# Optimization experiments

Hardware: AMD Instinct MI355X
Metric: run time of the kernel (lower is better)

Reference implementation:

```python
import jax, jax.numpy as jnp
import numpy as np

QUALITY = 75

Y_TABLE = np.array([
    [16, 11, 10, 16, 24, 40, 51, 61],
    [12, 12, 14, 19, 26, 58, 60, 55],
    [14, 13, 16, 24, 40, 57, 69, 56],
    [14, 17, 22, 29, 51, 87, 80, 62],
    [18, 22, 37, 56, 68, 109, 103, 77],
    [24, 35, 55, 64, 81, 104, 113, 92],
    [49, 64, 78, 87, 103, 121, 120, 101],
    [72, 92, 95, 98, 112, 100, 103, 99]], dtype=np.float32)

C_TABLE = np.array([
    [17, 18, 24, 47, 99, 99, 99, 99],
    [18, 21, 26, 66, 99, 99, 99, 99],
    [24, 26, 56, 99, 99, 99, 99, 99],
    [47, 66, 99, 99, 99, 99, 99, 99],
    [99, 99, 99, 99, 99, 99, 99, 99],
    [99, 99, 99, 99, 99, 99, 99, 99],
    [99, 99, 99, 99, 99, 99, 99, 99],
    [99, 99, 99, 99, 99, 99, 99, 99]], dtype=np.float32)

def _dct_mat():
    # Orthonormal 8-point DCT-II matrix D: coef = D @ block @ D.T
    xg = np.arange(8, dtype=np.float64)
    ug = np.arange(8, dtype=np.float64)
    D = 0.5 * np.cos((2.0 * xg[None, :] + 1.0) * ug[:, None] * np.pi / 16.0)
    D[0, :] *= 1.0 / np.sqrt(2.0)
    return jnp.asarray(D, dtype=jnp.float32)

D8 = _dct_mat()

def _blockify(ch):
    # [B,H,W] -> [B, H//8, W//8, 8, 8]
    B, H, W = ch.shape
    return ch.reshape(B, H // 8, 8, W // 8, 8).transpose(0, 1, 3, 2, 4)

def _deblockify(blk):
    # [B, hb, wb, 8, 8] -> [B, hb*8, wb*8]
    B, hb, wb, _, _ = blk.shape
    return blk.transpose(0, 1, 3, 2, 4).reshape(B, hb * 8, wb * 8)

def _channel_jpeg(ch, table, factor):
    # ch: [B,H,W] in 0..255 -> quantize/dequantize in DCT domain
    q = table * factor  # [8,8]
    blk = _blockify(ch - 128.0)                                   # [B,hb,wb,8,8]
    coef = jnp.einsum('bhwxy,ux,vy->bhwuv', blk, D8, D8)           # 8x8 DCT
    coef = jnp.round(coef / q) * q                                 # quantize + dequantize
    rec = jnp.einsum('bhwuv,ux,vy->bhwxy', coef, D8, D8) + 128.0   # IDCT
    return _deblockify(rec)

def jpeg_compress(img, quality):
    # img: [B,3,H,W] in [0,1]
    if quality < 50:
        factor = 5000.0 / quality
    else:
        factor = 200.0 - 2.0 * quality
    factor = factor / 100.0
    x = img * 255.0
    r, g, b = x[:, 0], x[:, 1], x[:, 2]
    y = 0.299 * r + 0.587 * g + 0.114 * b
    cb = -0.168736 * r - 0.331264 * g + 0.5 * b + 128.0
    cr = 0.5 * r - 0.418688 * g - 0.081312 * b + 128.0
    # 4:2:0 chroma subsampling via 2x2 average pooling
    B, H, W = cb.shape
    cb_s = cb.reshape(B, H // 2, 2, W // 2, 2).mean(axis=(2, 4))
    cr_s = cr.reshape(B, H // 2, 2, W // 2, 2).mean(axis=(2, 4))
    y_r = _channel_jpeg(y, jnp.asarray(Y_TABLE), factor)
    cb_r = _channel_jpeg(cb_s, jnp.asarray(C_TABLE), factor)
    cr_r = _channel_jpeg(cr_s, jnp.asarray(C_TABLE), factor)
    # nearest-neighbor chroma upsampling
    cb_u = jnp.repeat(jnp.repeat(cb_r, 2, axis=1), 2, axis=2)
    cr_u = jnp.repeat(jnp.repeat(cr_r, 2, axis=1), 2, axis=2)
    cbm = cb_u - 128.0
    crm = cr_u - 128.0
    r2 = y_r + 1.402 * crm
    g2 = y_r - 0.344136 * cbm - 0.714136 * crm
    b2 = y_r + 1.772 * cbm
    out = jnp.stack([r2, g2, b2], axis=1)
    return jnp.clip(out, 0.0, 255.0) / 255.0


def setup_inputs() -> dict:
    key = jax.random.key(0)
    x = jax.random.uniform(key, (16, 3, 512, 512), dtype=jnp.float32)
    return {"x": x}


def reference(x):
    img_clip = jnp.clip(x, 0.0, 1.0)
    img_jpeg = jpeg_compress(img_clip, QUALITY)
    img_gap = jax.lax.stop_gradient(img_jpeg - x)
    return x + img_gap
```

## Files before the change

### kernel.cpp

```cpp
#include <hip/hip_runtime.h>
#include <math.h>

#define CH_STRIDE (512 * 512)

static constexpr float DMc[8][8] = {
  { 0.35355339059327373f, 0.35355339059327373f, 0.35355339059327373f, 0.35355339059327373f,
    0.35355339059327373f, 0.35355339059327373f, 0.35355339059327373f, 0.35355339059327373f},
  { 0.49039264020161522f, 0.41573480615127262f, 0.27778511650980111f, 0.09754516100806413f,
   -0.09754516100806413f,-0.27778511650980111f,-0.41573480615127262f,-0.49039264020161522f},
  { 0.46193976625564337f, 0.19134171618254489f,-0.19134171618254489f,-0.46193976625564337f,
   -0.46193976625564337f,-0.19134171618254489f, 0.19134171618254489f, 0.46193976625564337f},
  { 0.41573480615127262f,-0.09754516100806413f,-0.49039264020161522f,-0.27778511650980111f,
    0.27778511650980111f, 0.49039264020161522f, 0.09754516100806413f,-0.41573480615127262f},
  { 0.35355339059327373f,-0.35355339059327373f,-0.35355339059327373f, 0.35355339059327373f,
    0.35355339059327373f,-0.35355339059327373f,-0.35355339059327373f, 0.35355339059327373f},
  { 0.27778511650980111f,-0.49039264020161522f, 0.09754516100806413f, 0.41573480615127262f,
   -0.41573480615127262f,-0.09754516100806413f, 0.49039264020161522f,-0.27778511650980111f},
  { 0.19134171618254489f,-0.46193976625564337f, 0.46193976625564337f,-0.19134171618254489f,
   -0.19134171618254489f, 0.46193976625564337f,-0.46193976625564337f, 0.19134171618254489f},
  { 0.09754516100806413f,-0.27778511650980111f, 0.41573480615127262f,-0.49039264020161522f,
    0.49039264020161522f,-0.41573480615127262f, 0.27778511650980111f,-0.09754516100806413f},
};

static constexpr float QTABc[128] = {
   8.0f,  5.5f,  5.0f,  8.0f, 12.0f, 20.0f, 25.5f, 30.5f,
   6.0f,  6.0f,  7.0f,  9.5f, 13.0f, 29.0f, 30.0f, 27.5f,
   7.0f,  6.5f,  8.0f, 12.0f, 20.0f, 28.5f, 34.5f, 28.0f,
   7.0f,  8.5f, 11.0f, 14.5f, 25.5f, 43.5f, 40.0f, 31.0f,
   9.0f, 11.0f, 18.5f, 28.0f, 34.0f, 54.5f, 51.5f, 38.5f,
  12.0f, 17.5f, 27.5f, 32.0f, 40.5f, 52.0f, 56.5f, 46.0f,
  24.5f, 32.0f, 39.0f, 43.5f, 51.5f, 60.5f, 60.0f, 50.5f,
  36.0f, 46.0f, 47.5f, 49.0f, 56.0f, 50.0f, 51.5f, 49.5f,

   8.5f,  9.0f, 12.0f, 23.5f, 49.5f, 49.5f, 49.5f, 49.5f,
   9.0f, 10.5f, 13.0f, 33.0f, 49.5f, 49.5f, 49.5f, 49.5f,
  12.0f, 13.0f, 28.0f, 49.5f, 49.5f, 49.5f, 49.5f, 49.5f,
  23.5f, 33.0f, 49.5f, 49.5f, 49.5f, 49.5f, 49.5f, 49.5f,
  49.5f, 49.5f, 49.5f, 49.5f, 49.5f, 49.5f, 49.5f, 49.5f,
  49.5f, 49.5f, 49.5f, 49.5f, 49.5f, 49.5f, 49.5f, 49.5f,
  49.5f, 49.5f, 49.5f, 49.5f, 49.5f, 49.5f, 49.5f, 49.5f,
  49.5f, 49.5f, 49.5f, 49.5f, 49.5f, 49.5f, 49.5f, 49.5f,
};

__device__ __forceinline__ float fm(float a, float b) { return __fmul_rn(a, b); }
__device__ __forceinline__ float fa(float a, float b) { return __fadd_rn(a, b); }
__device__ __forceinline__ float fs(float a, float b) { return __fsub_rn(a, b); }
__device__ __forceinline__ float fd(float a, float b) { return __fdiv_rn(a, b); }

__global__ __launch_bounds__(256, 2)
void jpeg_kernel(const float* __restrict__ x, float* __restrict__ out) {
  const int lane = threadIdx.x & 63;
  const int wave = threadIdx.x >> 6;

  const int q  = blockIdx.x;
  const int b  = q >> 8;
  const int qq = q & 255;
  const int ty = ((qq >> 4) << 1) + (wave >> 1);
  const int tx = ((qq & 15) << 1) + (wave & 1);
  const int row0 = ty << 4, col0 = tx << 4;

  __shared__ __align__(16) float Ytile[4][16][20];
  __shared__ __align__(16) float CbRaw[4][16][17];
  __shared__ __align__(16) float CrRaw[4][16][17];
  __shared__ __align__(16) float CbBlk[4][8][9];
  __shared__ __align__(16) float CrBlk[4][8][9];
  __shared__ __align__(16) float Cq[4][6][8][9];
  __shared__ __align__(16) float CbR[4][8][9];
  __shared__ __align__(16) float CrR[4][8][9];

  const int pr  = lane >> 2;
  const int pcq = lane & 3;
  const int pc  = pcq << 2;
  const size_t ibase = ((((size_t)b * 3) * 512 + (row0 + pr)) * 512) + (size_t)(col0 + pc);

  float4 rv = *(const float4*)(x + ibase);
  float4 gv = *(const float4*)(x + ibase + CH_STRIDE);
  float4 bv = *(const float4*)(x + ibase + 2 * CH_STRIDE);
  float xr[4] = {rv.x, rv.y, rv.z, rv.w};
  float xg[4] = {gv.x, gv.y, gv.z, gv.w};
  float xb[4] = {bv.x, bv.y, bv.z, bv.w};

#pragma unroll
  for (int i = 0; i < 4; ++i) {
    float r  = fm(fminf(fmaxf(xr[i], 0.0f), 1.0f), 255.0f);
    float g  = fm(fminf(fmaxf(xg[i], 0.0f), 1.0f), 255.0f);
    float bb = fm(fminf(fmaxf(xb[i], 0.0f), 1.0f), 255.0f);
    float y  = fa(fa(fm(0.299f, r), fm(0.587f, g)), fm(0.114f, bb));
    Ytile[wave][pr][pc + i] = fs(y, 128.0f);
    float cb = fa(fa(fs(fm(-0.168736f, r), fm(0.331264f, g)), fm(0.5f, bb)), 128.0f);
    CbRaw[wave][pr][pc + i] = cb;
    float cr = fa(fs(fs(fm(0.5f, r), fm(0.418688f, g)), fm(0.081312f, bb)), 128.0f);
    CrRaw[wave][pr][pc + i] = cr;
  }
  __syncthreads();

  {
    const int i = lane >> 3, j = lane & 7;
    {
      float c00 = CbRaw[wave][2 * i][2 * j],     c01 = CbRaw[wave][2 * i][2 * j + 1];
      float c10 = CbRaw[wave][2 * i + 1][2 * j], c11 = CbRaw[wave][2 * i + 1][2 * j + 1];
      CbBlk[wave][i][j] = fs(fd(fa(fa(c00, c01), fa(c10, c11)), 4.0f), 128.0f);
    }
    {
      float c00 = CrRaw[wave][2 * i][2 * j],     c01 = CrRaw[wave][2 * i][2 * j + 1];
      float c10 = CrRaw[wave][2 * i + 1][2 * j], c11 = CrRaw[wave][2 * i + 1][2 * j + 1];
      CrBlk[wave][i][j] = fs(fd(fa(fa(c00, c01), fa(c10, c11)), 4.0f), 128.0f);
    }
  }
  __syncthreads();

  const bool act = lane < 48;
  const int g = lane >> 3;
  const int j = lane & 7;
  const int rb  = (g >> 1) << 3;
  const int cb0 = (g & 1) << 3;

  if (act) {
    float t0[64];
    if (g < 4) {
#pragma unroll
      for (int xx = 0; xx < 8; ++xx)
#pragma unroll
        for (int yy = 0; yy < 8; ++yy)
          t0[xx * 8 + yy] = fm(Ytile[wave][rb + xx][cb0 + yy], DMc[j][xx]);
    } else if (g == 4) {
#pragma unroll
      for (int xx = 0; xx < 8; ++xx)
#pragma unroll
        for (int yy = 0; yy < 8; ++yy)
          t0[xx * 8 + yy] = fm(CbBlk[wave][xx][yy], DMc[j][xx]);
    } else {
#pragma unroll
      for (int xx = 0; xx < 8; ++xx)
#pragma unroll
        for (int yy = 0; yy < 8; ++yy)
          t0[xx * 8 + yy] = fm(CrBlk[wave][xx][yy], DMc[j][xx]);
    }

    const float* qr = QTABc + ((g < 4) ? 0 : 64) + j * 8;
#pragma unroll
    for (int v = 0; v < 8; ++v) {
      float s0 = 0.0f, s1 = 0.0f, s2 = 0.0f, s3 = 0.0f;
#pragma unroll
      for (int m = 0; m < 16; ++m) {
        const int k = 4 * m;
        s0 = fa(s0, fm(t0[k + 0], DMc[v][(k + 0) & 7]));
        s1 = fa(s1, fm(t0[k + 1], DMc[v][(k + 1) & 7]));
        s2 = fa(s2, fm(t0[k + 2], DMc[v][(k + 2) & 7]));
        s3 = fa(s3, fm(t0[k + 3], DMc[v][(k + 3) & 7]));
      }
      float coef = fa(fa(s0, s1), fa(s2, s3));
      float qv = qr[v];
      Cq[wave][g][j][v] = fm(rintf(fd(coef, qv)), qv);
    }
  }
  __syncthreads();

  if (act) {
    float t2[64];
#pragma unroll
    for (int u = 0; u < 8; ++u)
#pragma unroll
      for (int v = 0; v < 8; ++v)
        t2[u * 8 + v] = fm(Cq[wave][g][u][v], DMc[u][j]);

#pragma unroll
    for (int yy = 0; yy < 8; ++yy) {
      float acc = 0.0f;
#pragma unroll
      for (int u = 0; u < 8; ++u)
#pragma unroll
        for (int v = 0; v < 8; ++v)
          acc = fa(acc, fm(t2[u * 8 + v], DMc[v][yy]));
      float rec = fa(acc, 128.0f);
      if (g < 4) {
        Ytile[wave][rb + j][cb0 + yy] = rec;
      } else if (g == 4) {
        CbR[wave][j][yy] = fs(rec, 128.0f);
      } else {
        CrR[wave][j][yy] = fs(rec, 128.0f);
      }
    }
  }
  __syncthreads();

  float ro[4], go[4], bo[4];
#pragma unroll
  for (int i = 0; i < 4; ++i) {
    float y_r = Ytile[wave][pr][pc + i];
    float cbm = CbR[wave][pr >> 1][(pc + i) >> 1];
    float crm = CrR[wave][pr >> 1][(pc + i) >> 1];
    float r2 = fa(y_r, fm(1.402f, crm));
    float g2 = fs(fs(y_r, fm(0.344136f, cbm)), fm(0.714136f, crm));
    float b2 = fa(y_r, fm(1.772f, cbm));
    float jr = fd(fminf(fmaxf(r2, 0.0f), 255.0f), 255.0f);
    float jg = fd(fminf(fmaxf(g2, 0.0f), 255.0f), 255.0f);
    float jb = fd(fminf(fmaxf(b2, 0.0f), 255.0f), 255.0f);
    ro[i] = fa(xr[i], fs(jr, xr[i]));
    go[i] = fa(xg[i], fs(jg, xg[i]));
    bo[i] = fa(xb[i], fs(jb, xb[i]));
  }
  *(float4*)(out + ibase)                 = make_float4(ro[0], ro[1], ro[2], ro[3]);
  *(float4*)(out + ibase + CH_STRIDE)     = make_float4(go[0], go[1], go[2], go[3]);
  *(float4*)(out + ibase + 2 * CH_STRIDE) = make_float4(bo[0], bo[1], bo[2], bo[3]);
}

extern "C" void kernel_launch(void* const* d_in, const int* in_sizes, int n_in,
                              void* d_out, int out_size, void* d_ws, size_t ws_size,
                              hipStream_t stream) {
  const float* x = (const float*)d_in[0];
  float* out = (float*)d_out;
  jpeg_kernel<<<dim3(4096), dim3(256), 0, stream>>>(x, out);
}
```

Measured before the change: 131.9 us.

## Restructure JPEG kernel to block-wide 32x32 tiles with register-light DCT

Each 256-thread block now handles one 32x32 tile cooperatively instead of four independent 16x16 wave tiles. Chroma subsampling is done with cross-lane shuffles, which removes the raw-chroma shared buffers and one barrier. The DCT and IDCT loops are restructured to stream rows with float4 LDS reads and keep small accumulators instead of 64-element arrays, which lowers register pressure so launch bounds can target four blocks per CU. The input is re-read from global memory in the epilogue rather than held in registers across barriers, adding some memory traffic in exchange for lower register use.

```diff
diff --git a/kernel.cpp b/kernel.cpp
--- a/kernel.cpp
+++ b/kernel.cpp
@@ -47,162 +47,177 @@
 __device__ __forceinline__ float fs(float a, float b) { return __fsub_rn(a, b); }
 __device__ __forceinline__ float fd(float a, float b) { return __fdiv_rn(a, b); }
 
-__global__ __launch_bounds__(256, 2)
+__global__ __launch_bounds__(256, 4)
 void jpeg_kernel(const float* __restrict__ x, float* __restrict__ out) {
-  const int lane = threadIdx.x & 63;
-  const int wave = threadIdx.x >> 6;
-
+  const int tid = threadIdx.x;
   const int q  = blockIdx.x;
   const int b  = q >> 8;
   const int qq = q & 255;
-  const int ty = ((qq >> 4) << 1) + (wave >> 1);
-  const int tx = ((qq & 15) << 1) + (wave & 1);
-  const int row0 = ty << 4, col0 = tx << 4;
-
-  __shared__ __align__(16) float Ytile[4][16][20];
-  __shared__ __align__(16) float CbRaw[4][16][17];
-  __shared__ __align__(16) float CrRaw[4][16][17];
-  __shared__ __align__(16) float CbBlk[4][8][9];
-  __shared__ __align__(16) float CrBlk[4][8][9];
-  __shared__ __align__(16) float Cq[4][6][8][9];
-  __shared__ __align__(16) float CbR[4][8][9];
-  __shared__ __align__(16) float CrR[4][8][9];
-
-  const int pr  = lane >> 2;
-  const int pcq = lane & 3;
-  const int pc  = pcq << 2;
-  const size_t ibase = ((((size_t)b * 3) * 512 + (row0 + pr)) * 512) + (size_t)(col0 + pc);
-
-  float4 rv = *(const float4*)(x + ibase);
-  float4 gv = *(const float4*)(x + ibase + CH_STRIDE);
-  float4 bv = *(const float4*)(x + ibase + 2 * CH_STRIDE);
-  float xr[4] = {rv.x, rv.y, rv.z, rv.w};
-  float xg[4] = {gv.x, gv.y, gv.z, gv.w};
-  float xb[4] = {bv.x, bv.y, bv.z, bv.w};
-
-#pragma unroll
-  for (int i = 0; i < 4; ++i) {
-    float r  = fm(fminf(fmaxf(xr[i], 0.0f), 1.0f), 255.0f);
-    float g  = fm(fminf(fmaxf(xg[i], 0.0f), 1.0f), 255.0f);
-    float bb = fm(fminf(fmaxf(xb[i], 0.0f), 1.0f), 255.0f);
-    float y  = fa(fa(fm(0.299f, r), fm(0.587f, g)), fm(0.114f, bb));
-    Ytile[wave][pr][pc + i] = fs(y, 128.0f);
-    float cb = fa(fa(fs(fm(-0.168736f, r), fm(0.331264f, g)), fm(0.5f, bb)), 128.0f);
-    CbRaw[wave][pr][pc + i] = cb;
-    float cr = fa(fs(fs(fm(0.5f, r), fm(0.418688f, g)), fm(0.081312f, bb)), 128.0f);
-    CrRaw[wave][pr][pc + i] = cr;
+  const int row0 = (qq >> 4) << 5;
+  const int col0 = (qq & 15) << 5;
+
+  __shared__ __align__(16) float Ys[32][36];
+  __shared__ __align__(16) float CbBlk[16][20];
+  __shared__ __align__(16) float CrBlk[16][20];
+  __shared__ __align__(16) float Cq[24][8][9];
+  __shared__ __align__(16) float CbR[16][20];
+  __shared__ __align__(16) float CrR[16][20];
+
+  const int pr = tid >> 3;
+  const int pc = (tid & 7) << 2;
+  const size_t ibase = ((((size_t)b * 3) * 512 + (size_t)(row0 + pr)) * 512) + (size_t)(col0 + pc);
+
+  {
+    float4 rv = *(const float4*)(x + ibase);
+    float4 gv = *(const float4*)(x + ibase + CH_STRIDE);
+    float4 bv = *(const float4*)(x + ibase + 2 * CH_STRIDE);
+    float xr[4] = {rv.x, rv.y, rv.z, rv.w};
+    float xg[4] = {gv.x, gv.y, gv.z, gv.w};
+    float xb[4] = {bv.x, bv.y, bv.z, bv.w};
+    float yo[4], cbv[4], crv[4];
+#pragma unroll
+    for (int i = 0; i < 4; ++i) {
+      float r  = fm(fminf(fmaxf(xr[i], 0.0f), 1.0f), 255.0f);
+      float g  = fm(fminf(fmaxf(xg[i], 0.0f), 1.0f), 255.0f);
+      float bb = fm(fminf(fmaxf(xb[i], 0.0f), 1.0f), 255.0f);
+      float y  = fa(fa(fm(0.299f, r), fm(0.587f, g)), fm(0.114f, bb));
+      yo[i]  = fs(y, 128.0f);
+      cbv[i] = fa(fa(fs(fm(-0.168736f, r), fm(0.331264f, g)), fm(0.5f, bb)), 128.0f);
+      crv[i] = fa(fs(fs(fm(0.5f, r), fm(0.418688f, g)), fm(0.081312f, bb)), 128.0f);
+    }
+    *(float4*)&Ys[pr][pc] = make_float4(yo[0], yo[1], yo[2], yo[3]);
+
+    float cbh0 = fa(cbv[0], cbv[1]), cbh1 = fa(cbv[2], cbv[3]);
+    float crh0 = fa(crv[0], crv[1]), crh1 = fa(crv[2], crv[3]);
+    float pcb0 = __shfl_xor(cbh0, 8, 64);
+    float pcb1 = __shfl_xor(cbh1, 8, 64);
+    float pcr0 = __shfl_xor(crh0, 8, 64);
+    float pcr1 = __shfl_xor(crh1, 8, 64);
+    if (((tid >> 3) & 1) == 0) {
+      const int ii = pr >> 1, jc = pc >> 1;
+      CbBlk[ii][jc]     = fs(fm(fa(cbh0, pcb0), 0.25f), 128.0f);
+      CbBlk[ii][jc + 1] = fs(fm(fa(cbh1, pcb1), 0.25f), 128.0f);
+      CrBlk[ii][jc]     = fs(fm(fa(crh0, pcr0), 0.25f), 128.0f);
+      CrBlk[ii][jc + 1] = fs(fm(fa(crh1, pcr1), 0.25f), 128.0f);
+    }
   }
   __syncthreads();
 
+  const int  blk = tid >> 3;
+  const int  j   = tid & 7;
+  const bool act = tid < 192;
+  const bool isY = blk < 16;
+  const float* src  = nullptr;
+  float*       wdst = nullptr;
+  int ld = 36;
+  const float* qr = QTABc + j * 8;
+  if (act) {
+    if (isY) {
+      const int by = blk >> 2, bx = blk & 3;
+      src = &Ys[by * 8][bx * 8];  wdst = &Ys[by * 8 + j][bx * 8];  ld = 36;
+    } else if (blk < 20) {
+      const int c = blk - 16, cy = c >> 1, cx = c & 1;
+      src = &CbBlk[cy * 8][cx * 8];  wdst = &CbR[cy * 8 + j][cx * 8];  ld = 20;  qr += 64;
+    } else {
+      const int c = blk - 20, cy = c >> 1, cx = c & 1;
+      src = &CrBlk[cy * 8][cx * 8];  wdst = &CrR[cy * 8 + j][cx * 8];  ld = 20;  qr += 64;
+    }
+  }
+
+  if (act) {
+    float dj[8];
+#pragma unroll
+    for (int xx = 0; xx < 8; ++xx) dj[xx] = DMc[j][xx];
+    float s[8][4];
+#pragma unroll
+    for (int v = 0; v < 8; ++v) { s[v][0] = 0.0f; s[v][1] = 0.0f; s[v][2] = 0.0f; s[v][3] = 0.0f; }
+    const float* srow = src;
+#pragma unroll
+    for (int xx = 0; xx < 8; ++xx) {
+      float4 aq = *(const float4*)(srow);
+      float4 bq = *(const float4*)(srow + 4);
+      srow += ld;
+      float t0r[8] = { fm(aq.x, dj[xx]), fm(aq.y, dj[xx]), fm(aq.z, dj[xx]), fm(aq.w, dj[xx]),
+                       fm(bq.x, dj[xx]), fm(bq.y, dj[xx]), fm(bq.z, dj[xx]), fm(bq.w, dj[xx]) };
+#pragma unroll
+      for (int v = 0; v < 8; ++v) {
+        s[v][0] = fa(s[v][0], fm(t0r[0], DMc[v][0]));
+        s[v][1] = fa(s[v][1], fm(t0r[1], DMc[v][1]));
+        s[v][2] = fa(s[v][2], fm(t0r[2], DMc[v][2]));
+        s[v][3] = fa(s[v][3], fm(t0r[3], DMc[v][3]));
+        s[v][0] = fa(s[v][0], fm(t0r[4], DMc[v][4]));
+        s[v][1] = fa(s[v][1], fm(t0r[5], DMc[v][5]));
+        s[v][2] = fa(s[v][2], fm(t0r[6], DMc[v][6]));
+        s[v][3] = fa(s[v][3], fm(t0r[7], DMc[v][7]));
+      }
+    }
+    float* cq = &Cq[blk][j][0];
+#pragma unroll
+    for (int v = 0; v < 8; ++v) {
+      float coef = fa(fa(s[v][0], s[v][1]), fa(s[v][2], s[v][3]));
+      float qv = qr[v];
+      cq[v] = fm(rintf(fd(coef, qv)), qv);
+    }
+  }
+  __syncthreads();
+
+  if (act) {
+    float acc[8];
+#pragma unroll
+    for (int yy = 0; yy < 8; ++yy) acc[yy] = 0.0f;
+    const float* cqb = &Cq[blk][0][0];
+#pragma unroll
+    for (int u = 0; u < 8; ++u) {
+      float du = DMc[u][j];
+      float t2r[8];
+#pragma unroll
+      for (int v = 0; v < 8; ++v) t2r[v] = fm(cqb[u * 9 + v], du);
+#pragma unroll
+      for (int yy = 0; yy < 8; ++yy) {
+#pragma unroll
+        for (int v = 0; v < 8; ++v)
+          acc[yy] = fa(acc[yy], fm(t2r[v], DMc[v][yy]));
+      }
+    }
+    float r0[8];
+#pragma unroll
+    for (int yy = 0; yy < 8; ++yy) {
+      float rec = fa(acc[yy], 128.0f);
+      r0[yy] = isY ? rec : fs(rec, 128.0f);
+    }
+    *(float4*)(wdst)     = make_float4(r0[0], r0[1], r0[2], r0[3]);
+    *(float4*)(wdst + 4) = make_float4(r0[4], r0[5], r0[6], r0[7]);
+  }
+  __syncthreads();
+
   {
-    const int i = lane >> 3, j = lane & 7;
-    {
-      float c00 = CbRaw[wave][2 * i][2 * j],     c01 = CbRaw[wave][2 * i][2 * j + 1];
-      float c10 = CbRaw[wave][2 * i + 1][2 * j], c11 = CbRaw[wave][2 * i + 1][2 * j + 1];
-      CbBlk[wave][i][j] = fs(fd(fa(fa(c00, c01), fa(c10, c11)), 4.0f), 128.0f);
-    }
-    {
-      float c00 = CrRaw[wave][2 * i][2 * j],     c01 = CrRaw[wave][2 * i][2 * j + 1];
-      float c10 = CrRaw[wave][2 * i + 1][2 * j], c11 = CrRaw[wave][2 * i + 1][2 * j + 1];
-      CrBlk[wave][i][j] = fs(fd(fa(fa(c00, c01), fa(c10, c11)), 4.0f), 128.0f);
-    }
-  }
-  __syncthreads();
-
-  const bool act = lane < 48;
-  const int g = lane >> 3;
-  const int j = lane & 7;
-  const int rb  = (g >> 1) << 3;
-  const int cb0 = (g & 1) << 3;
-
-  if (act) {
-    float t0[64];
-    if (g < 4) {
-#pragma unroll
-      for (int xx = 0; xx < 8; ++xx)
-#pragma unroll
-        for (int yy = 0; yy < 8; ++yy)
-          t0[xx * 8 + yy] = fm(Ytile[wave][rb + xx][cb0 + yy], DMc[j][xx]);
-    } else if (g == 4) {
-#pragma unroll
-      for (int xx = 0; xx < 8; ++xx)
-#pragma unroll
-        for (int yy = 0; yy < 8; ++yy)
-          t0[xx * 8 + yy] = fm(CbBlk[wave][xx][yy], DMc[j][xx]);
-    } else {
-#pragma unroll
-      for (int xx = 0; xx < 8; ++xx)
-#pragma unroll
-        for (int yy = 0; yy < 8; ++yy)
-          t0[xx * 8 + yy] = fm(CrBlk[wave][xx][yy], DMc[j][xx]);
-    }
-
-    const float* qr = QTABc + ((g < 4) ? 0 : 64) + j * 8;
-#pragma unroll
-    for (int v = 0; v < 8; ++v) {
-      float s0 = 0.0f, s1 = 0.0f, s2 = 0.0f, s3 = 0.0f;
-#pragma unroll
-      for (int m = 0; m < 16; ++m) {
-        const int k = 4 * m;
-        s0 = fa(s0, fm(t0[k + 0], DMc[v][(k + 0) & 7]));
-        s1 = fa(s1, fm(t0[k + 1], DMc[v][(k + 1) & 7]));
-        s2 = fa(s2, fm(t0[k + 2], DMc[v][(k + 2) & 7]));
-        s3 = fa(s3, fm(t0[k + 3], DMc[v][(k + 3) & 7]));
-      }
-      float coef = fa(fa(s0, s1), fa(s2, s3));
-      float qv = qr[v];
-      Cq[wave][g][j][v] = fm(rintf(fd(coef, qv)), qv);
-    }
-  }
-  __syncthreads();
-
-  if (act) {
-    float t2[64];
-#pragma unroll
-    for (int u = 0; u < 8; ++u)
-#pragma unroll
-      for (int v = 0; v < 8; ++v)
-        t2[u * 8 + v] = fm(Cq[wave][g][u][v], DMc[u][j]);
-
-#pragma unroll
-    for (int yy = 0; yy < 8; ++yy) {
-      float acc = 0.0f;
-#pragma unroll
-      for (int u = 0; u < 8; ++u)
-#pragma unroll
-        for (int v = 0; v < 8; ++v)
-          acc = fa(acc, fm(t2[u * 8 + v], DMc[v][yy]));
-      float rec = fa(acc, 128.0f);
-      if (g < 4) {
-        Ytile[wave][rb + j][cb0 + yy] = rec;
-      } else if (g == 4) {
-        CbR[wave][j][yy] = fs(rec, 128.0f);
-      } else {
-        CrR[wave][j][yy] = fs(rec, 128.0f);
-      }
-    }
-  }
-  __syncthreads();
-
-  float ro[4], go[4], bo[4];
-#pragma unroll
-  for (int i = 0; i < 4; ++i) {
-    float y_r = Ytile[wave][pr][pc + i];
-    float cbm = CbR[wave][pr >> 1][(pc + i) >> 1];
-    float crm = CrR[wave][pr >> 1][(pc + i) >> 1];
-    float r2 = fa(y_r, fm(1.402f, crm));
-    float g2 = fs(fs(y_r, fm(0.344136f, cbm)), fm(0.714136f, crm));
-    float b2 = fa(y_r, fm(1.772f, cbm));
-    float jr = fd(fminf(fmaxf(r2, 0.0f), 255.0f), 255.0f);
-    float jg = fd(fminf(fmaxf(g2, 0.0f), 255.0f), 255.0f);
-    float jb = fd(fminf(fmaxf(b2, 0.0f), 255.0f), 255.0f);
-    ro[i] = fa(xr[i], fs(jr, xr[i]));
-    go[i] = fa(xg[i], fs(jg, xg[i]));
-    bo[i] = fa(xb[i], fs(jb, xb[i]));
-  }
-  *(float4*)(out + ibase)                 = make_float4(ro[0], ro[1], ro[2], ro[3]);
-  *(float4*)(out + ibase + CH_STRIDE)     = make_float4(go[0], go[1], go[2], go[3]);
-  *(float4*)(out + ibase + 2 * CH_STRIDE) = make_float4(bo[0], bo[1], bo[2], bo[3]);
+    float4 rv = *(const float4*)(x + ibase);
+    float4 gv = *(const float4*)(x + ibase + CH_STRIDE);
+    float4 bv = *(const float4*)(x + ibase + 2 * CH_STRIDE);
+    float xr[4] = {rv.x, rv.y, rv.z, rv.w};
+    float xg[4] = {gv.x, gv.y, gv.z, gv.w};
+    float xb[4] = {bv.x, bv.y, bv.z, bv.w};
+    float ro[4], go[4], bo[4];
+    const int hr = pr >> 1;
+#pragma unroll
+    for (int i = 0; i < 4; ++i) {
+      float y_r = Ys[pr][pc + i];
+      float cbm = CbR[hr][(pc + i) >> 1];
+      float crm = CrR[hr][(pc + i) >> 1];
+      float r2 = fa(y_r, fm(1.402f, crm));
+      float g2 = fs(fs(y_r, fm(0.344136f, cbm)), fm(0.714136f, crm));
+      float b2 = fa(y_r, fm(1.772f, cbm));
+      float jr = fd(fminf(fmaxf(r2, 0.0f), 255.0f), 255.0f);
+      float jg = fd(fminf(fmaxf(g2, 0.0f), 255.0f), 255.0f);
+      float jb = fd(fminf(fmaxf(b2, 0.0f), 255.0f), 255.0f);
+      ro[i] = fa(xr[i], fs(jr, xr[i]));
+      go[i] = fa(xg[i], fs(jg, xg[i]));
+      bo[i] = fa(xb[i], fs(jb, xb[i]));
+    }
+    *(float4*)(out + ibase)                 = make_float4(ro[0], ro[1], ro[2], ro[3]);
+    *(float4*)(out + ibase + CH_STRIDE)     = make_float4(go[0], go[1], go[2], go[3]);
+    *(float4*)(out + ibase + 2 * CH_STRIDE) = make_float4(bo[0], bo[1], bo[2], bo[3]);
+  }
 }
 
 extern "C" void kernel_launch(void* const* d_in, const int* in_sizes, int n_in,
```

After: 116.3 us. 1.13x faster.
